# Kernel optimization log

Hardware: AMD Instinct MI355X
Metric: run time of the kernel (lower is better)

The kernel has to match this reference:

```python
import jax, jax.numpy as jnp
import numpy as np

N_SRC1, N_DST1, N_DST2 = 200000, 50000, 10000
E1, E2 = 2000000, 400000
IN_F, H_F, N_CLS = 128, 256, 47


def setup_inputs() -> dict:
    key = jax.random.key(0)
    ks = jax.random.split(key, 10)
    x = jax.random.normal(ks[0], (N_SRC1, IN_F), dtype=jnp.float32)
    W_self1 = jax.random.normal(ks[1], (IN_F, H_F), dtype=jnp.float32) * (1.0 / np.sqrt(IN_F))
    W_neigh1 = jax.random.normal(ks[2], (IN_F, H_F), dtype=jnp.float32) * (1.0 / np.sqrt(IN_F))
    b1 = jnp.zeros((H_F,), dtype=jnp.float32)
    W_self2 = jax.random.normal(ks[3], (H_F, N_CLS), dtype=jnp.float32) * (1.0 / np.sqrt(H_F))
    W_neigh2 = jax.random.normal(ks[4], (H_F, N_CLS), dtype=jnp.float32) * (1.0 / np.sqrt(H_F))
    b2 = jnp.zeros((N_CLS,), dtype=jnp.float32)
    src1 = jax.random.randint(ks[5], (E1,), 0, N_SRC1, dtype=jnp.int64)
    dst1 = jnp.sort(jax.random.randint(ks[6], (E1,), 0, N_DST1, dtype=jnp.int64))
    src2 = jax.random.randint(ks[7], (E2,), 0, N_DST1, dtype=jnp.int64)
    dst2 = jnp.sort(jax.random.randint(ks[8], (E2,), 0, N_DST2, dtype=jnp.int64))
    return {"x": x, "W_self1": W_self1, "W_neigh1": W_neigh1, "b1": b1,
            "W_self2": W_self2, "W_neigh2": W_neigh2, "b2": b2,
            "src1": src1, "dst1": dst1, "src2": src2, "dst2": dst2,
            "n_dst1": N_DST1, "n_dst2": N_DST2}


def _sage_mean(h_src, h_dst, src, dst, n_dst, W_self, W_neigh, b):
    # mean neighbor aggregation: gather src feats, segment-sum onto dst, divide by in-degree
    msum = jax.ops.segment_sum(h_src[src], dst, num_segments=n_dst)  # [n_dst, F]
    deg = jax.ops.segment_sum(jnp.ones(src.shape, h_src.dtype), dst, num_segments=n_dst)
    h_neigh = msum / jnp.maximum(deg, 1.0)[:, None]
    return h_dst @ W_self + h_neigh @ W_neigh + b


def reference(x, W_self1, W_neigh1, b1, W_self2, W_neigh2, b2,
              src1, dst1, src2, dst2, n_dst1, n_dst2):
    # layer 1 (dst nodes are the prefix of src nodes, DGL MFG convention)
    h = _sage_mean(x, x[:n_dst1], src1, dst1, n_dst1, W_self1, W_neigh1, b1)
    h = jax.nn.relu(h)  # dropout = identity (eval mode)
    # layer 2
    out = _sage_mean(h, h[:n_dst2], src2, dst2, n_dst2, W_self2, W_neigh2, b2)
    return out
```

## Files before the change

### kernel.cpp

```cpp
#include <hip/hip_runtime.h>

constexpr int N_DST1 = 50000;
constexpr int N_DST2 = 10000;
constexpr int E1     = 2000000;
constexpr int E2     = 400000;
constexpr int IN_F   = 128;
constexpr int H_F    = 256;
constexpr int N_CLS  = 47;

constexpr size_t RP1_OFF = 0;
constexpr size_t RP2_OFF = 204800;
constexpr size_t BPS_OFF = 245760;
constexpr size_t BPN_OFF = 311296;
constexpr size_t BP2_OFF = 376832;
constexpr size_t X8_OFF  = 430080;
constexpr size_t HN1_OFF = 26030080;
constexpr size_t HB_OFF  = 38830080;
constexpr size_t Y_OFF   = 64430080;
constexpr size_t YAGG_OFF= 77230080;

using f32x4  = __attribute__((ext_vector_type(4))) float;
using f32x2  = __attribute__((ext_vector_type(2))) float;
using short8 = __attribute__((ext_vector_type(8))) short;

__device__ __forceinline__ ushort f2bf(float f) {
    union { float f; unsigned u; } v; v.f = f;
    unsigned u = v.u;
    return (ushort)((u + 0x7fffu + ((u >> 16) & 1u)) >> 16);
}

__device__ __forceinline__ float bflo(unsigned x) {
    union { unsigned q; float f; } w; w.q = x << 16; return w.f;
}
__device__ __forceinline__ float bfhi(unsigned x) {
    union { unsigned q; float f; } w; w.q = x & 0xffff0000u; return w.f;
}

constexpr int CAST_BLKS = 200000 * IN_F / 8 / 256;
constexpr int PACK_BLKS = 44;
constexpr int RP_BLKS   = (N_DST1 + N_DST2 + 2 + 255) / 256;

__global__ __launch_bounds__(256) void setup_all(
    const float* __restrict__ x, unsigned char* __restrict__ x8,
    const float* __restrict__ Ws1, const float* __restrict__ Wn1,
    const float* __restrict__ Ws2, const float* __restrict__ Wn2,
    ushort* __restrict__ bps, ushort* __restrict__ bpn, ushort* __restrict__ bp2,
    const int* __restrict__ dst1, const int* __restrict__ dst2,
    int* __restrict__ rp1, int* __restrict__ rp2) {
    int b = blockIdx.x;
    if (b < CAST_BLKS) {
        int i = b * 256 + threadIdx.x;
        float4 v0 = ((const float4*)x)[2 * i];
        float4 v1 = ((const float4*)x)[2 * i + 1];
        int p0 = __builtin_amdgcn_cvt_pk_fp8_f32(v0.x, v0.y, 0, false);
        p0     = __builtin_amdgcn_cvt_pk_fp8_f32(v0.z, v0.w, p0, true);
        int p1 = __builtin_amdgcn_cvt_pk_fp8_f32(v1.x, v1.y, 0, false);
        p1     = __builtin_amdgcn_cvt_pk_fp8_f32(v1.z, v1.w, p1, true);
        uint2 o; o.x = (unsigned)p0; o.y = (unsigned)p1;
        ((uint2*)x8)[i] = o;
    } else if (b < CAST_BLKS + PACK_BLKS) {
        int pb = b - CAST_BLKS;
        if (pb < 32) {
            const float* W = (pb < 16) ? Ws1 : Wn1;
            ushort* P      = (pb < 16) ? bps : bpn;
            int idx = (pb & 15) * 256 + threadIdx.x;
            int lane = idx & 63, kb = (idx >> 6) & 3, nb = idx >> 8;
            int n  = nb * 16 + (lane & 15);
            int k0 = kb * 32 + ((lane >> 4) * 8);
            ushort tmp[8];
#pragma unroll
            for (int j = 0; j < 8; ++j) tmp[j] = f2bf(W[(k0 + j) * H_F + n]);
            ((uint4*)P)[idx] = *(uint4*)tmp;
        } else {
            int idx = (pb - 32) * 256 + threadIdx.x;
            if (idx < 3072) {
                int lane = idx & 63, rem = idx >> 6;
                int nb = rem % 3, kb = rem / 3;
                int col = nb * 16 + (lane & 15);
                int k0  = (kb & 7) * 32 + ((lane >> 4) * 8);
                const float* W = (kb < 8) ? Ws2 : Wn2;
                ushort tmp[8];
#pragma unroll
                for (int j = 0; j < 8; ++j)
                    tmp[j] = (col < N_CLS) ? f2bf(W[(k0 + j) * N_CLS + col]) : (ushort)0;
                ((uint4*)bp2)[(kb * 3 + nb) * 64 + lane] = *(uint4*)tmp;
            }
        }
    } else {
        int idx = (b - CAST_BLKS - PACK_BLKS) * 256 + threadIdx.x;
        const int* dst; int* rp; int E; int target;
        if (idx <= N_DST1) { dst = dst1; rp = rp1; E = E1; target = idx; }
        else if (idx <= N_DST1 + 1 + N_DST2) {
            dst = dst2; rp = rp2; E = E2; target = idx - (N_DST1 + 1);
        } else return;
        int lo = 0, hi = E;
        while (lo < hi) {
            int mid = (lo + hi) >> 1;
            if (dst[mid] < target) lo = mid + 1; else hi = mid;
        }
        rp[target] = lo;
    }
}

__global__ __launch_bounds__(256) void agg1b(const unsigned char* __restrict__ x8,
                                             const int* __restrict__ src,
                                             const int* __restrict__ rp,
                                             ushort* __restrict__ hn) {
    int t = threadIdx.x & 63;
    int d = blockIdx.x * 4 + (threadIdx.x >> 6);
    int s = rp[d], e = rp[d + 1];
    int deg = e - s;
    const uint4* x4 = (const uint4*)x8;
    int g = t >> 3, c = t & 7;
    f32x2 a2[8] = {};
    auto accv = [&](uint4 v) {
        a2[0] += __builtin_amdgcn_cvt_pk_f32_fp8((int)v.x, false);
        a2[1] += __builtin_amdgcn_cvt_pk_f32_fp8((int)v.x, true);
        a2[2] += __builtin_amdgcn_cvt_pk_f32_fp8((int)v.y, false);
        a2[3] += __builtin_amdgcn_cvt_pk_f32_fp8((int)v.y, true);
        a2[4] += __builtin_amdgcn_cvt_pk_f32_fp8((int)v.z, false);
        a2[5] += __builtin_amdgcn_cvt_pk_f32_fp8((int)v.z, true);
        a2[6] += __builtin_amdgcn_cvt_pk_f32_fp8((int)v.w, false);
        a2[7] += __builtin_amdgcn_cvt_pk_f32_fp8((int)v.w, true);
    };
    for (int b0 = s; b0 < e; b0 += 64) {
        int nb = min(64, e - b0);
        int idx = 0;
        if (t < nb) idx = src[b0 + t];
        int nfull = nb >> 3;
        int j = 0;
        for (; j + 4 <= nfull; j += 4) {
            int e0 = __shfl(idx, (j + 0) * 8 + g);
            int e1 = __shfl(idx, (j + 1) * 8 + g);
            int e2 = __shfl(idx, (j + 2) * 8 + g);
            int e3 = __shfl(idx, (j + 3) * 8 + g);
            uint4 v0 = x4[(size_t)e0 * 8 + c];
            uint4 v1 = x4[(size_t)e1 * 8 + c];
            uint4 v2 = x4[(size_t)e2 * 8 + c];
            uint4 v3 = x4[(size_t)e3 * 8 + c];
            accv(v0); accv(v1); accv(v2); accv(v3);
        }
        for (; j < nfull; ++j) {
            int e0 = __shfl(idx, j * 8 + g);
            uint4 v = x4[(size_t)e0 * 8 + c];
            accv(v);
        }
        int rem = nb & 7;
        int er = __shfl(idx, (nfull * 8 + g) & 63);
        if (g < rem) {
            uint4 v = x4[(size_t)er * 8 + c];
            accv(v);
        }
    }
#pragma unroll
    for (int q = 0; q < 8; ++q) {
#pragma unroll
        for (int h = 0; h < 2; ++h) {
            float av = a2[q][h];
            av += __shfl_xor(av, 8);
            av += __shfl_xor(av, 16);
            av += __shfl_xor(av, 32);
            a2[q][h] = av;
        }
    }
    if (t < 8) {
        float inv = 1.f / fmaxf((float)deg, 1.f);
        unsigned o[8];
#pragma unroll
        for (int p = 0; p < 8; ++p)
            o[p] = (unsigned)f2bf(a2[p][0] * inv) |
                   ((unsigned)f2bf(a2[p][1] * inv) << 16);
        uint4* hrow = (uint4*)hn + (size_t)d * 16 + t * 2;
        hrow[0] = make_uint4(o[0], o[1], o[2], o[3]);
        hrow[1] = make_uint4(o[4], o[5], o[6], o[7]);
    }
}

__global__ __launch_bounds__(256) void gemm1_mfma(
    const float* __restrict__ x, const ushort* __restrict__ hn1,
    const ushort* __restrict__ BpS, const ushort* __restrict__ BpN,
    const ushort* __restrict__ P2, const float* __restrict__ b1,
    ushort* __restrict__ hb, ushort* __restrict__ y) {
    __shared__ ushort lh[16][264];
    __shared__ f32x4 pred[3][3][64];
    int tid = threadIdx.x;
    int wave = tid >> 6, lane = tid & 63;
    int m0 = blockIdx.x * 16;
    int nb0 = wave * 4;
    int mloc = lane & 15;
    int mrow = m0 + mloc;
    int koff = (lane >> 4) * 8;

    const float*  Af = x   + (size_t)mrow * IN_F;
    const ushort* Ah = hn1 + (size_t)mrow * IN_F;
    short8 a0[4], a1[4];
#pragma unroll
    for (int kb = 0; kb < 4; ++kb) {
        float4 q0 = *(const float4*)(Af + kb * 32 + koff);
        float4 q1 = *(const float4*)(Af + kb * 32 + koff + 4);
        a0[kb][0] = (short)f2bf(q0.x); a0[kb][1] = (short)f2bf(q0.y);
        a0[kb][2] = (short)f2bf(q0.z); a0[kb][3] = (short)f2bf(q0.w);
        a0[kb][4] = (short)f2bf(q1.x); a0[kb][5] = (short)f2bf(q1.y);
        a0[kb][6] = (short)f2bf(q1.z); a0[kb][7] = (short)f2bf(q1.w);
        a1[kb] = *(const short8*)(Ah + kb * 32 + koff);
    }

    f32x4 acc[4];
#pragma unroll
    for (int nb = 0; nb < 4; ++nb) acc[nb] = (f32x4){0.f, 0.f, 0.f, 0.f};

#pragma unroll
    for (int kb = 0; kb < 4; ++kb)
#pragma unroll
        for (int nb = 0; nb < 4; ++nb) {
            short8 b = *(const short8*)(BpS + ((size_t)((nb0 + nb) * 4 + kb) * 64 + lane) * 8);
            acc[nb] = __builtin_amdgcn_mfma_f32_16x16x32_bf16(a0[kb], b, acc[nb], 0, 0, 0);
        }
#pragma unroll
    for (int kb = 0; kb < 4; ++kb)
#pragma unroll
        for (int nb = 0; nb < 4; ++nb) {
            short8 b = *(const short8*)(BpN + ((size_t)((nb0 + nb) * 4 + kb) * 64 + lane) * 8);
            acc[nb] = __builtin_amdgcn_mfma_f32_16x16x32_bf16(a1[kb], b, acc[nb], 0, 0, 0);
        }

    int crow0 = (lane >> 4) * 4;
    int ccol  = lane & 15;
#pragma unroll
    for (int nb = 0; nb < 4; ++nb) {
        size_t col = (size_t)(nb0 + nb) * 16 + ccol;
        float bias = b1[col];
#pragma unroll
        for (int r = 0; r < 4; ++r) {
            int row = crow0 + r;
            float v = fmaxf(acc[nb][r] + bias, 0.f);
            ushort bv = f2bf(v);
            lh[row][col] = bv;
            if (m0 + row < N_DST2) hb[(size_t)(m0 + row) * H_F + col] = bv;
        }
    }
    __syncthreads();

    f32x4 acc2[3];
#pragma unroll
    for (int q = 0; q < 3; ++q) acc2[q] = (f32x4){0.f, 0.f, 0.f, 0.f};
#pragma unroll
    for (int i = 0; i < 2; ++i) {
        int kb = wave * 2 + i;
        short8 a = *(const short8*)&lh[mloc][kb * 32 + koff];
#pragma unroll
        for (int q = 0; q < 3; ++q) {
            short8 b = *(const short8*)(P2 + ((size_t)((8 + kb) * 3 + q) * 64 + lane) * 8);
            acc2[q] = __builtin_amdgcn_mfma_f32_16x16x32_bf16(a, b, acc2[q], 0, 0, 0);
        }
    }
    if (wave != 0) {
#pragma unroll
        for (int q = 0; q < 3; ++q) pred[wave - 1][q][lane] = acc2[q];
    }
    __syncthreads();
    if (wave == 0) {
#pragma unroll
        for (int q = 0; q < 3; ++q) {
            f32x4 v = acc2[q];
            v += pred[0][q][lane]; v += pred[1][q][lane]; v += pred[2][q][lane];
#pragma unroll
            for (int r = 0; r < 4; ++r)
                y[(size_t)(m0 + crow0 + r) * 64 + q * 16 + ccol] = f2bf(v[r]);
        }
#pragma unroll
        for (int r = 0; r < 4; ++r)
            y[(size_t)(m0 + crow0 + r) * 64 + 48 + ccol] = 0;
    }
}

__global__ __launch_bounds__(256) void agg2y(const ushort* __restrict__ y,
                                             const int* __restrict__ src,
                                             const int* __restrict__ rp,
                                             float* __restrict__ yagg) {
    int t = threadIdx.x & 63;
    int d = blockIdx.x * 4 + (threadIdx.x >> 6);
    int s = rp[d], e = rp[d + 1];
    int deg = e - s;
    const uint4* y4 = (const uint4*)y;
    int g = t >> 3, c = t & 7;
    float a[8] = {};
    auto accv = [&](uint4 v) {
        a[0] += bflo(v.x); a[1] += bfhi(v.x);
        a[2] += bflo(v.y); a[3] += bfhi(v.y);
        a[4] += bflo(v.z); a[5] += bfhi(v.z);
        a[6] += bflo(v.w); a[7] += bfhi(v.w);
    };
    for (int b0 = s; b0 < e; b0 += 64) {
        int nb = min(64, e - b0);
        int idx = 0;
        if (t < nb) idx = src[b0 + t];
        int nfull = nb >> 3;
        int j = 0;
        for (; j + 4 <= nfull; j += 4) {
            int e0 = __shfl(idx, (j + 0) * 8 + g);
            int e1 = __shfl(idx, (j + 1) * 8 + g);
            int e2 = __shfl(idx, (j + 2) * 8 + g);
            int e3 = __shfl(idx, (j + 3) * 8 + g);
            uint4 v0 = y4[(size_t)e0 * 8 + c];
            uint4 v1 = y4[(size_t)e1 * 8 + c];
            uint4 v2 = y4[(size_t)e2 * 8 + c];
            uint4 v3 = y4[(size_t)e3 * 8 + c];
            accv(v0); accv(v1); accv(v2); accv(v3);
        }
        for (; j < nfull; ++j) {
            int e0 = __shfl(idx, j * 8 + g);
            uint4 v = y4[(size_t)e0 * 8 + c];
            accv(v);
        }
        int rem = nb & 7;
        int er = __shfl(idx, (nfull * 8 + g) & 63);
        if (g < rem) {
            uint4 v = y4[(size_t)er * 8 + c];
            accv(v);
        }
    }
#pragma unroll
    for (int q = 0; q < 8; ++q) {
        float av = a[q];
        av += __shfl_xor(av, 8);
        av += __shfl_xor(av, 16);
        av += __shfl_xor(av, 32);
        a[q] = av;
    }
    if (t < 8) {
        float inv = 1.f / fmaxf((float)deg, 1.f);
        float4 o0 = make_float4(a[0] * inv, a[1] * inv, a[2] * inv, a[3] * inv);
        float4 o1 = make_float4(a[4] * inv, a[5] * inv, a[6] * inv, a[7] * inv);
        float4* row = (float4*)(yagg + (size_t)d * 64 + t * 8);
        row[0] = o0;
        row[1] = o1;
    }
}

__global__ __launch_bounds__(256) void gemm2_mfma(
    const ushort* __restrict__ hb, const float* __restrict__ yagg,
    const ushort* __restrict__ P2, const float* __restrict__ b2,
    float* __restrict__ out) {
    int tid = threadIdx.x;
    int wave = tid >> 6, lane = tid & 63;
    int m0 = (blockIdx.x * 4 + wave) * 16;
    if (m0 >= N_DST2) return;
    int mrow = m0 + (lane & 15);
    int koff = (lane >> 4) * 8;

    f32x4 acc[3];
#pragma unroll
    for (int nb = 0; nb < 3; ++nb) acc[nb] = (f32x4){0.f, 0.f, 0.f, 0.f};

#pragma unroll
    for (int kb = 0; kb < 8; ++kb) {
        short8 a = *(const short8*)(hb + (size_t)mrow * H_F + kb * 32 + koff);
#pragma unroll
        for (int nb = 0; nb < 3; ++nb) {
            short8 b = *(const short8*)(P2 + ((size_t)(kb * 3 + nb) * 64 + lane) * 8);
            acc[nb] = __builtin_amdgcn_mfma_f32_16x16x32_bf16(a, b, acc[nb], 0, 0, 0);
        }
    }
    int crow0 = m0 + (lane >> 4) * 4;
    int ccol  = lane & 15;
#pragma unroll
    for (int nb = 0; nb < 3; ++nb) {
        int col = nb * 16 + ccol;
        if (col < N_CLS) {
            float bias = b2[col];
#pragma unroll
            for (int r = 0; r < 4; ++r) {
                float nv = yagg[(size_t)(crow0 + r) * 64 + col];
                out[(size_t)(crow0 + r) * N_CLS + col] = acc[nb][r] + nv + bias;
            }
        }
    }
}

extern "C" void kernel_launch(void* const* d_in, const int* in_sizes, int n_in,
                              void* d_out, int out_size, void* d_ws, size_t ws_size,
                              hipStream_t stream) {
    const float* x   = (const float*)d_in[0];
    const float* Ws1 = (const float*)d_in[1];
    const float* Wn1 = (const float*)d_in[2];
    const float* b1  = (const float*)d_in[3];
    const float* Ws2 = (const float*)d_in[4];
    const float* Wn2 = (const float*)d_in[5];
    const float* b2  = (const float*)d_in[6];
    const int* src1  = (const int*)d_in[7];
    const int* dst1  = (const int*)d_in[8];
    const int* src2  = (const int*)d_in[9];
    const int* dst2  = (const int*)d_in[10];
    float* out = (float*)d_out;

    char* ws = (char*)d_ws;
    int*           rp1 = (int*)(ws + RP1_OFF);
    int*           rp2 = (int*)(ws + RP2_OFF);
    ushort*        bps = (ushort*)(ws + BPS_OFF);
    ushort*        bpn = (ushort*)(ws + BPN_OFF);
    ushort*        bp2 = (ushort*)(ws + BP2_OFF);
    unsigned char* x8  = (unsigned char*)(ws + X8_OFF);
    ushort*        hn1 = (ushort*)(ws + HN1_OFF);
    ushort*        hb  = (ushort*)(ws + HB_OFF);
    ushort*        y   = (ushort*)(ws + Y_OFF);
    float*         yagg= (float*)(ws + YAGG_OFF);

    setup_all<<<CAST_BLKS + PACK_BLKS + RP_BLKS, 256, 0, stream>>>(
        x, x8, Ws1, Wn1, Ws2, Wn2, bps, bpn, bp2, dst1, dst2, rp1, rp2);
    agg1b<<<N_DST1 / 4, 256, 0, stream>>>(x8, src1, rp1, hn1);
    gemm1_mfma<<<N_DST1 / 16, 256, 0, stream>>>(x, hn1, bps, bpn, bp2, b1, hb, y);
    agg2y<<<N_DST2 / 4, 256, 0, stream>>>(y, src2, rp2, yagg);
    gemm2_mfma<<<(N_DST2 / 16 + 3) / 4, 256, 0, stream>>>(hb, yagg, bp2, b2, out);
}
```

Baseline: 276.0 us.

## Fuse layer-2 self GEMM into gemm1 and finish output in agg2y

The layer-2 self projection (h @ W_self2) now runs inside gemm1 for the first N_DST2 rows, from the hidden tile already in shared memory, and is written to a small float z buffer. The final bias add, mean scaling and self-term sum move into the layer-2 aggregation epilogue. This removes the gemm2 kernel launch and the hb and yagg round trips through global memory. In exchange, gemm1 blocks that own early rows do extra MFMAs and use more shared memory, and the output is written with scalar strided stores.

```diff
diff --git a/kernel.cpp b/kernel.cpp
--- a/kernel.cpp
+++ b/kernel.cpp
@@ -15,9 +15,8 @@
 constexpr size_t BP2_OFF = 376832;
 constexpr size_t X8_OFF  = 430080;
 constexpr size_t HN1_OFF = 26030080;
-constexpr size_t HB_OFF  = 38830080;
-constexpr size_t Y_OFF   = 64430080;
-constexpr size_t YAGG_OFF= 77230080;
+constexpr size_t Y_OFF   = 38830080;
+constexpr size_t ZS_OFF  = 45230080;
 
 using f32x4  = __attribute__((ext_vector_type(4))) float;
 using f32x2  = __attribute__((ext_vector_type(2))) float;
@@ -180,9 +179,9 @@
     const float* __restrict__ x, const ushort* __restrict__ hn1,
     const ushort* __restrict__ BpS, const ushort* __restrict__ BpN,
     const ushort* __restrict__ P2, const float* __restrict__ b1,
-    ushort* __restrict__ hb, ushort* __restrict__ y) {
+    ushort* __restrict__ y, float* __restrict__ z) {
     __shared__ ushort lh[16][264];
-    __shared__ f32x4 pred[3][3][64];
+    __shared__ f32x4 pred[3][6][64];
     int tid = threadIdx.x;
     int wave = tid >> 6, lane = tid & 63;
     int m0 = blockIdx.x * 16;
@@ -190,6 +189,7 @@
     int mloc = lane & 15;
     int mrow = m0 + mloc;
     int koff = (lane >> 4) * 8;
+    bool zb = (m0 < N_DST2);
 
     const float*  Af = x   + (size_t)mrow * IN_F;
     const ushort* Ah = hn1 + (size_t)mrow * IN_F;
@@ -234,35 +234,47 @@
         for (int r = 0; r < 4; ++r) {
             int row = crow0 + r;
             float v = fmaxf(acc[nb][r] + bias, 0.f);
-            ushort bv = f2bf(v);
-            lh[row][col] = bv;
-            if (m0 + row < N_DST2) hb[(size_t)(m0 + row) * H_F + col] = bv;
+            lh[row][col] = f2bf(v);
         }
     }
     __syncthreads();
 
-    f32x4 acc2[3];
-#pragma unroll
-    for (int q = 0; q < 3; ++q) acc2[q] = (f32x4){0.f, 0.f, 0.f, 0.f};
+    f32x4 accY[3], accZ[3];
+#pragma unroll
+    for (int q = 0; q < 3; ++q) {
+        accY[q] = (f32x4){0.f, 0.f, 0.f, 0.f};
+        accZ[q] = (f32x4){0.f, 0.f, 0.f, 0.f};
+    }
 #pragma unroll
     for (int i = 0; i < 2; ++i) {
         int kb = wave * 2 + i;
         short8 a = *(const short8*)&lh[mloc][kb * 32 + koff];
 #pragma unroll
         for (int q = 0; q < 3; ++q) {
-            short8 b = *(const short8*)(P2 + ((size_t)((8 + kb) * 3 + q) * 64 + lane) * 8);
-            acc2[q] = __builtin_amdgcn_mfma_f32_16x16x32_bf16(a, b, acc2[q], 0, 0, 0);
+            short8 bn = *(const short8*)(P2 + ((size_t)((8 + kb) * 3 + q) * 64 + lane) * 8);
+            accY[q] = __builtin_amdgcn_mfma_f32_16x16x32_bf16(a, bn, accY[q], 0, 0, 0);
+        }
+        if (zb) {
+#pragma unroll
+            for (int q = 0; q < 3; ++q) {
+                short8 bs = *(const short8*)(P2 + ((size_t)(kb * 3 + q) * 64 + lane) * 8);
+                accZ[q] = __builtin_amdgcn_mfma_f32_16x16x32_bf16(a, bs, accZ[q], 0, 0, 0);
+            }
         }
     }
     if (wave != 0) {
 #pragma unroll
-        for (int q = 0; q < 3; ++q) pred[wave - 1][q][lane] = acc2[q];
+        for (int q = 0; q < 3; ++q) pred[wave - 1][q][lane] = accY[q];
+        if (zb) {
+#pragma unroll
+            for (int q = 0; q < 3; ++q) pred[wave - 1][3 + q][lane] = accZ[q];
+        }
     }
     __syncthreads();
     if (wave == 0) {
 #pragma unroll
         for (int q = 0; q < 3; ++q) {
-            f32x4 v = acc2[q];
+            f32x4 v = accY[q];
             v += pred[0][q][lane]; v += pred[1][q][lane]; v += pred[2][q][lane];
 #pragma unroll
             for (int r = 0; r < 4; ++r)
@@ -271,13 +283,26 @@
 #pragma unroll
         for (int r = 0; r < 4; ++r)
             y[(size_t)(m0 + crow0 + r) * 64 + 48 + ccol] = 0;
+        if (zb) {
+#pragma unroll
+            for (int q = 0; q < 3; ++q) {
+                f32x4 v = accZ[q];
+                v += pred[0][3 + q][lane]; v += pred[1][3 + q][lane];
+                v += pred[2][3 + q][lane];
+#pragma unroll
+                for (int r = 0; r < 4; ++r)
+                    z[(size_t)(m0 + crow0 + r) * 64 + q * 16 + ccol] = v[r];
+            }
+        }
     }
 }
 
 __global__ __launch_bounds__(256) void agg2y(const ushort* __restrict__ y,
                                              const int* __restrict__ src,
                                              const int* __restrict__ rp,
-                                             float* __restrict__ yagg) {
+                                             const float* __restrict__ z,
+                                             const float* __restrict__ b2,
+                                             float* __restrict__ out) {
     int t = threadIdx.x & 63;
     int d = blockIdx.x * 4 + (threadIdx.x >> 6);
     int s = rp[d], e = rp[d + 1];
@@ -330,50 +355,12 @@
     }
     if (t < 8) {
         float inv = 1.f / fmaxf((float)deg, 1.f);
-        float4 o0 = make_float4(a[0] * inv, a[1] * inv, a[2] * inv, a[3] * inv);
-        float4 o1 = make_float4(a[4] * inv, a[5] * inv, a[6] * inv, a[7] * inv);
-        float4* row = (float4*)(yagg + (size_t)d * 64 + t * 8);
-        row[0] = o0;
-        row[1] = o1;
-    }
-}
-
-__global__ __launch_bounds__(256) void gemm2_mfma(
-    const ushort* __restrict__ hb, const float* __restrict__ yagg,
-    const ushort* __restrict__ P2, const float* __restrict__ b2,
-    float* __restrict__ out) {
-    int tid = threadIdx.x;
-    int wave = tid >> 6, lane = tid & 63;
-    int m0 = (blockIdx.x * 4 + wave) * 16;
-    if (m0 >= N_DST2) return;
-    int mrow = m0 + (lane & 15);
-    int koff = (lane >> 4) * 8;
-
-    f32x4 acc[3];
-#pragma unroll
-    for (int nb = 0; nb < 3; ++nb) acc[nb] = (f32x4){0.f, 0.f, 0.f, 0.f};
-
-#pragma unroll
-    for (int kb = 0; kb < 8; ++kb) {
-        short8 a = *(const short8*)(hb + (size_t)mrow * H_F + kb * 32 + koff);
-#pragma unroll
-        for (int nb = 0; nb < 3; ++nb) {
-            short8 b = *(const short8*)(P2 + ((size_t)(kb * 3 + nb) * 64 + lane) * 8);
-            acc[nb] = __builtin_amdgcn_mfma_f32_16x16x32_bf16(a, b, acc[nb], 0, 0, 0);
-        }
-    }
-    int crow0 = m0 + (lane >> 4) * 4;
-    int ccol  = lane & 15;
-#pragma unroll
-    for (int nb = 0; nb < 3; ++nb) {
-        int col = nb * 16 + ccol;
-        if (col < N_CLS) {
-            float bias = b2[col];
-#pragma unroll
-            for (int r = 0; r < 4; ++r) {
-                float nv = yagg[(size_t)(crow0 + r) * 64 + col];
-                out[(size_t)(crow0 + r) * N_CLS + col] = acc[nb][r] + nv + bias;
-            }
+        const float* zr = z + (size_t)d * 64 + t * 8;
+#pragma unroll
+        for (int p = 0; p < 8; ++p) {
+            int col = t * 8 + p;
+            if (col < N_CLS)
+                out[(size_t)d * N_CLS + col] = a[p] * inv + zr[p] + b2[col];
         }
     }
 }
@@ -402,14 +389,12 @@
     ushort*        bp2 = (ushort*)(ws + BP2_OFF);
     unsigned char* x8  = (unsigned char*)(ws + X8_OFF);
     ushort*        hn1 = (ushort*)(ws + HN1_OFF);
-    ushort*        hb  = (ushort*)(ws + HB_OFF);
     ushort*        y   = (ushort*)(ws + Y_OFF);
-    float*         yagg= (float*)(ws + YAGG_OFF);
+    float*         z   = (float*)(ws + ZS_OFF);
 
     setup_all<<<CAST_BLKS + PACK_BLKS + RP_BLKS, 256, 0, stream>>>(
         x, x8, Ws1, Wn1, Ws2, Wn2, bps, bpn, bp2, dst1, dst2, rp1, rp2);
     agg1b<<<N_DST1 / 4, 256, 0, stream>>>(x8, src1, rp1, hn1);
-    gemm1_mfma<<<N_DST1 / 16, 256, 0, stream>>>(x, hn1, bps, bpn, bp2, b1, hb, y);
-    agg2y<<<N_DST2 / 4, 256, 0, stream>>>(y, src2, rp2, yagg);
-    gemm2_mfma<<<(N_DST2 / 16 + 3) / 4, 256, 0, stream>>>(hb, yagg, bp2, b2, out);
-}
+    gemm1_mfma<<<N_DST1 / 16, 256, 0, stream>>>(x, hn1, bps, bpn, bp2, b1, y, z);
+    agg2y<<<N_DST2 / 4, 256, 0, stream>>>(y, src2, rp2, z, b2, out);
+}
```

After: 279.5 us. Within noise of the previous version (+1.3%).
